# Performance work log

Measured on AMD Instinct MI355X. Metric: run time of the kernel, lower is better.

Reference implementation:

```python
import jax, jax.numpy as jnp
import numpy as np

IN_FEATURES = 8192
OUT_FEATURES = 28672
BATCH = 8  # tokens; skinny GEMM -> memory-bound weight streaming


def setup_inputs() -> dict:
    key = jax.random.key(0)
    k1, k2, k3, k4 = jax.random.split(key, 4)
    x = jax.random.normal(k1, (BATCH, IN_FEATURES), dtype=jnp.float32)
    # ternary codes in {0,1,2} -> weight values {-1,0,+1}; pack 4 codes / byte
    codes = jax.random.randint(k2, (OUT_FEATURES, IN_FEATURES), 0, 3, dtype=jnp.int32)
    codes4 = codes.reshape(OUT_FEATURES, IN_FEATURES // 4, 4)
    shifts = jnp.array([0, 2, 4, 6], dtype=jnp.int32)
    packed_weight = jnp.sum(codes4 << shifts, axis=-1).astype(jnp.int32)  # [O, I//4]
    weight_scale = jax.random.uniform(k3, (1,), dtype=jnp.float32, minval=0.01, maxval=0.1)
    bias = jax.random.normal(k4, (OUT_FEATURES,), dtype=jnp.float32)
    return {"x": x, "packed_weight": packed_weight, "weight_scale": weight_scale, "bias": bias}


def _unpack_ternary(packed):
    # [O, I//4] int -> [O, I] ternary in {-1,0,1}
    shifts = jnp.array([0, 2, 4, 6], dtype=jnp.int32)
    w = ((packed[:, :, None] >> shifts) & 3) - 1  # [O, I//4, 4]
    return w.reshape(packed.shape[0], -1)


def reference(x, packed_weight, weight_scale, bias):
    B = x.shape[0]
    x_flat = x.reshape(B, IN_FEATURES)
    # per-tensor absmax int8 activation quantization
    absmax = jnp.maximum(jnp.max(jnp.abs(x_flat)), 1e-5)
    act_scale = absmax / 127.0
    x_q = jnp.clip(jnp.round(x_flat / act_scale), -128, 127)  # int8 values, kept f32
    w = _unpack_ternary(packed_weight).astype(jnp.float32)  # [O, I]
    # fused dequant GEMM: integer-valued accumulation, single scalar scale
    acc = jnp.einsum('bi,oi->bo', x_q, w)  # exact in f32 (|acc| << 2^24)
    scale = weight_scale[0] * act_scale
    out = acc * scale + bias
    return out.reshape(B, OUT_FEATURES)
```

## Files before the change

kernel.cpp:

```cpp
#include <hip/hip_runtime.h>
#include <stdint.h>

#define O_FEATS 28672
#define I_FEATS 8192
#define BATCH 8

typedef int i32x4 __attribute__((ext_vector_type(4)));


static __device__ __forceinline__ int unpack4(uint32_t p) {
  uint32_t lo = p & 0x0Fu;
  uint32_t hi = (p >> 4) & 0x0Fu;
  uint32_t a = (lo * 0x41u) & 0x0303u;
  uint32_t b = (hi * 0x41u) & 0x0303u;
  return (int)(a | (b << 16));
}

__global__ void k_absmax(const float* __restrict__ x, uint32_t* __restrict__ ws) {
  __shared__ float red[4];
  int t = threadIdx.x;
  float4 v = ((const float4*)x)[blockIdx.x * 256 + t];
  float m = fmaxf(fmaxf(fabsf(v.x), fabsf(v.y)), fmaxf(fabsf(v.z), fabsf(v.w)));
#pragma unroll
  for (int off = 32; off; off >>= 1)
    m = fmaxf(m, __shfl_xor(m, off));
  if ((t & 63) == 0) red[t >> 6] = m;
  __syncthreads();
  if (t == 0)
    ws[16 + blockIdx.x] =
        __float_as_uint(fmaxf(fmaxf(red[0], red[1]), fmaxf(red[2], red[3])));
}

__global__ void k_quant(const float* __restrict__ x, uint32_t* __restrict__ ws) {
  __shared__ float s_amax;
  __shared__ int reds[4];
  int t = threadIdx.x;
  if (blockIdx.x >= 64) {
    int row = 8 + ((blockIdx.x - 64) >> 3), seg = blockIdx.x & 7;
    int k0 = seg * 1024 + t * 4;
    int S = k0 >> 6, g = (k0 >> 4) & 3, j = k0 & 15;
    ws[1024 + ((S * 1024 + (g * 16 + row) * 16 + j) >> 2)] = 0u;
    return;
  }
  int b = blockIdx.x >> 3, seg = blockIdx.x & 7;
  if (t < 64) {
    float m = __uint_as_float(ws[16 + t]);
#pragma unroll
    for (int off = 32; off; off >>= 1)
      m = fmaxf(m, __shfl_xor(m, off));
    if (t == 0) {
      float a = fmaxf(m, 1e-5f);
      s_amax = a;
      ws[0] = __float_as_uint(a);
    }
  }
  __syncthreads();
  float s = s_amax / 127.0f;
  float4 v = ((const float4*)(x + b * I_FEATS + seg * 1024))[t];
  int q0 = (int)fminf(fmaxf(rintf(v.x / s), -128.f), 127.f);
  int q1 = (int)fminf(fmaxf(rintf(v.y / s), -128.f), 127.f);
  int q2 = (int)fminf(fmaxf(rintf(v.z / s), -128.f), 127.f);
  int q3 = (int)fminf(fmaxf(rintf(v.w / s), -128.f), 127.f);
  uint32_t pk = (uint32_t)(q0 & 0xff) | ((uint32_t)(q1 & 0xff) << 8) |
                ((uint32_t)(q2 & 0xff) << 16) | ((uint32_t)(q3 & 0xff) << 24);
  {
    int k0 = seg * 1024 + t * 4;
    int S = k0 >> 6, g = (k0 >> 4) & 3, j = k0 & 15;
    ws[1024 + ((S * 1024 + (g * 16 + b) * 16 + j) >> 2)] = pk;
  }
  int s4 = q0 + q1 + q2 + q3;
#pragma unroll
  for (int off = 32; off; off >>= 1)
    s4 += __shfl_xor(s4, off);
  if ((t & 63) == 0) reds[t >> 6] = s4;
  __syncthreads();
  if (t == 0)
    ws[128 + blockIdx.x] = (uint32_t)(reds[0] + reds[1] + reds[2] + reds[3]);
}

__global__ void __launch_bounds__(256, 4)
k_gemm(const int* __restrict__ Wp, const float* __restrict__ wscale,
       const float* __restrict__ bias, const uint32_t* __restrict__ ws,
       float* __restrict__ out) {
  __shared__ int red[4][32][4];
  __shared__ int s_sumx[BATCH];
  __shared__ float s_scale;

  const int t = threadIdx.x;
  const int wave = t >> 6, lane = t & 63;

  if (t < 64) {
    int p = (int)ws[128 + t];
    p += __shfl_xor(p, 1);
    p += __shfl_xor(p, 2);
    p += __shfl_xor(p, 4);
    if ((t & 7) == 0) s_sumx[t >> 3] = p;
    if (t == 0) s_scale = (__uint_as_float(ws[0]) / 127.0f) * wscale[0];
  }

  const int o_base = blockIdx.x * 16;
  const int m = lane & 15, g = lane >> 4;

  const uint8_t* xqT = (const uint8_t*)(ws + 1024);
  const int4* ap = (const int4*)(xqT + (size_t)(wave * 32) * 1024 + lane * 16);
  const int4* wp = (const int4*)((const uint8_t*)Wp + (size_t)(o_base + m) * 8192 +
                                 wave * 2048 + g * 16);

  i32x4 acc = {0, 0, 0, 0};
  int4 abuf[4], bbuf[4];
#pragma unroll
  for (int i = 0; i < 4; ++i) {
    abuf[i] = ap[i * 64];
    bbuf[i] = wp[i * 4];
  }
#pragma unroll
  for (int s = 0; s < 32; ++s) {
    int4 a = abuf[s & 3];
    int4 b = bbuf[s & 3];
    if (s + 4 < 32) {
      abuf[s & 3] = ap[(s + 4) * 64];
      bbuf[s & 3] = wp[(s + 4) * 4];
    }
    i32x4 af, bf;
    af.x = a.x; af.y = a.y; af.z = a.z; af.w = a.w;
    bf.x = unpack4((uint32_t)b.x);
    bf.y = unpack4((uint32_t)b.y);
    bf.z = unpack4((uint32_t)b.z);
    bf.w = unpack4((uint32_t)b.w);
    acc = __builtin_amdgcn_mfma_i32_16x16x64_i8(af, bf, acc, 0, 0, 0);
  }

  if (lane < 32) {
#pragma unroll
    for (int r = 0; r < 4; ++r) red[wave][lane][r] = acc[r];
  }
  __syncthreads();

  if (t < 32) {
    const int n = t & 15;
    const int q = t >> 4;
    const int o = o_base + n;
    const float bo = bias[o];
#pragma unroll
    for (int r = 0; r < 4; ++r) {
      int mm = q * 4 + r;
      int tot = red[0][t][r] + red[1][t][r] + red[2][t][r] + red[3][t][r];
      out[mm * O_FEATS + o] = (float)(tot - s_sumx[mm]) * s_scale + bo;
    }
  }
}

extern "C" void kernel_launch(void* const* d_in, const int* in_sizes, int n_in,
                              void* d_out, int out_size, void* d_ws, size_t ws_size,
                              hipStream_t stream) {
  const float* x = (const float*)d_in[0];
  const int* pw = (const int*)d_in[1];
  const float* wscale = (const float*)d_in[2];
  const float* bias = (const float*)d_in[3];
  float* out = (float*)d_out;
  uint32_t* ws = (uint32_t*)d_ws;

  k_absmax<<<64, 256, 0, stream>>>(x, ws);
  k_quant<<<128, 256, 0, stream>>>(x, ws);
  k_gemm<<<O_FEATS / 16, 256, 0, stream>>>(pw, wscale, bias, ws, out);
}
```

Measured before the change: 327.8 us.

## Make GEMM persistent with async global-to-LDS double-buffered weight streaming

The GEMM now launches 256 persistent blocks instead of 1792. Each block walks 7 output tiles and streams weight rows into a double-buffered LDS area with global_load_lds. Activations are loaded into registers once per block and reused across tiles, and hand-written waitcnt/barrier asm overlaps the loads with the MFMA work. The cost is lower occupancy (launch bounds of 1, large LDS use, 32 int4 registers) and half the MFMA lanes fed zeros, with latency hiding left to the block's own pipeline.

After: 349.1 us. 6.5% more time.

```diff
diff --git a/kernel.cpp b/kernel.cpp
--- a/kernel.cpp
+++ b/kernel.cpp
@@ -4,8 +4,15 @@
 #define O_FEATS 28672
 #define I_FEATS 8192
 #define BATCH 8
+#define PITCH_WB 8208
+#define HALF_B (8 * PITCH_WB)
 
 typedef int i32x4 __attribute__((ext_vector_type(4)));
+
+#define BAR_VM16 asm volatile("s_waitcnt vmcnt(16)\n\ts_barrier" ::: "memory")
+#define BAR_VM0  asm volatile("s_waitcnt vmcnt(0)\n\ts_barrier" ::: "memory")
+#define BAR_LGKM asm volatile("s_waitcnt lgkmcnt(0)\n\ts_barrier" ::: "memory")
+#define BAR_ONLY asm volatile("s_barrier" ::: "memory")
 
 
 static __device__ __forceinline__ int unpack4(uint32_t p) {
@@ -78,10 +85,11 @@
     ws[128 + blockIdx.x] = (uint32_t)(reds[0] + reds[1] + reds[2] + reds[3]);
 }
 
-__global__ void __launch_bounds__(256, 4)
+__global__ void __launch_bounds__(256, 1)
 k_gemm(const int* __restrict__ Wp, const float* __restrict__ wscale,
        const float* __restrict__ bias, const uint32_t* __restrict__ ws,
        float* __restrict__ out) {
+  __shared__ uint32_t Wlds[2 * 8 * (PITCH_WB / 4)];
   __shared__ int red[4][32][4];
   __shared__ int s_sumx[BATCH];
   __shared__ float s_scale;
@@ -97,56 +105,102 @@
     if ((t & 7) == 0) s_sumx[t >> 3] = p;
     if (t == 0) s_scale = (__uint_as_float(ws[0]) / 127.0f) * wscale[0];
   }
-
-  const int o_base = blockIdx.x * 16;
-  const int m = lane & 15, g = lane >> 4;
+  __syncthreads();
+
+  const uint8_t* W8 = (const uint8_t*)Wp;
+  uint8_t* L8 = (uint8_t*)Wlds;
+
+  {
+    const uint8_t* gs = W8 + (size_t)(blockIdx.x * 16 + 2 * wave) * 8192 + lane * 16;
+    uint32_t* ld = (uint32_t*)(L8 + 2 * wave * PITCH_WB);
+#pragma unroll
+    for (int i = 0; i < 16; ++i)
+      __builtin_amdgcn_global_load_lds(
+          (const uint32_t*)(gs + i * 1024),
+          ld + ((i >> 3) * PITCH_WB + (i & 7) * 1024) / 4, 16, 0, 0);
+  }
 
   const uint8_t* xqT = (const uint8_t*)(ws + 1024);
-  const int4* ap = (const int4*)(xqT + (size_t)(wave * 32) * 1024 + lane * 16);
-  const int4* wp = (const int4*)((const uint8_t*)Wp + (size_t)(o_base + m) * 8192 +
-                                 wave * 2048 + g * 16);
-
-  i32x4 acc = {0, 0, 0, 0};
-  int4 abuf[4], bbuf[4];
-#pragma unroll
-  for (int i = 0; i < 4; ++i) {
-    abuf[i] = ap[i * 64];
-    bbuf[i] = wp[i * 4];
-  }
-#pragma unroll
-  for (int s = 0; s < 32; ++s) {
-    int4 a = abuf[s & 3];
-    int4 b = bbuf[s & 3];
-    if (s + 4 < 32) {
-      abuf[s & 3] = ap[(s + 4) * 64];
-      bbuf[s & 3] = wp[(s + 4) * 4];
-    }
-    i32x4 af, bf;
-    af.x = a.x; af.y = a.y; af.z = a.z; af.w = a.w;
-    bf.x = unpack4((uint32_t)b.x);
-    bf.y = unpack4((uint32_t)b.y);
-    bf.z = unpack4((uint32_t)b.z);
-    bf.w = unpack4((uint32_t)b.w);
-    acc = __builtin_amdgcn_mfma_i32_16x16x64_i8(af, bf, acc, 0, 0, 0);
-  }
-
-  if (lane < 32) {
-#pragma unroll
-    for (int r = 0; r < 4; ++r) red[wave][lane][r] = acc[r];
-  }
-  __syncthreads();
-
-  if (t < 32) {
-    const int n = t & 15;
-    const int q = t >> 4;
-    const int o = o_base + n;
-    const float bo = bias[o];
-#pragma unroll
-    for (int r = 0; r < 4; ++r) {
-      int mm = q * 4 + r;
-      int tot = red[0][t][r] + red[1][t][r] + red[2][t][r] + red[3][t][r];
-      out[mm * O_FEATS + o] = (float)(tot - s_sumx[mm]) * s_scale + bo;
-    }
+  int4 a[32];
+#pragma unroll
+  for (int s = 0; s < 32; ++s)
+    a[s] = *(const int4*)(xqT + (size_t)(wave * 32 + s) * 1024 + lane * 16);
+
+  const int r8 = lane & 7, g = lane >> 4;
+  const bool act0 = ((lane >> 3) & 1) == 0;
+
+  const uint8_t* fr0 = L8 + r8 * PITCH_WB + wave * 2048 + g * 16;
+  const uint8_t* fr1 = L8 + HALF_B + r8 * PITCH_WB + wave * 2048 + g * 16;
+
+  for (int i = 0; i < 7; ++i) {
+    i32x4 acc = {0, 0, 0, 0};
+
+    {
+      const uint8_t* gs =
+          W8 + (size_t)((blockIdx.x + 256 * i) * 16 + 8 + 2 * wave) * 8192 + lane * 16;
+      uint32_t* ld = (uint32_t*)(L8 + HALF_B + 2 * wave * PITCH_WB);
+#pragma unroll
+      for (int k = 0; k < 16; ++k)
+        __builtin_amdgcn_global_load_lds(
+            (const uint32_t*)(gs + k * 1024),
+            ld + ((k >> 3) * PITCH_WB + (k & 7) * 1024) / 4, 16, 0, 0);
+    }
+    BAR_VM16;
+#pragma unroll
+    for (int s = 0; s < 32; ++s) {
+      int4 bw = *(const int4*)(fr0 + s * 64);
+      i32x4 bf, af;
+      bf.x = act0 ? unpack4((uint32_t)bw.x) : 0;
+      bf.y = act0 ? unpack4((uint32_t)bw.y) : 0;
+      bf.z = act0 ? unpack4((uint32_t)bw.z) : 0;
+      bf.w = act0 ? unpack4((uint32_t)bw.w) : 0;
+      af.x = a[s].x; af.y = a[s].y; af.z = a[s].z; af.w = a[s].w;
+      acc = __builtin_amdgcn_mfma_i32_16x16x64_i8(af, bf, acc, 0, 0, 0);
+    }
+    BAR_LGKM;
+
+    if (i < 6) {
+      const uint8_t* gs =
+          W8 + (size_t)((blockIdx.x + 256 * (i + 1)) * 16 + 2 * wave) * 8192 + lane * 16;
+      uint32_t* ld = (uint32_t*)(L8 + 2 * wave * PITCH_WB);
+#pragma unroll
+      for (int k = 0; k < 16; ++k)
+        __builtin_amdgcn_global_load_lds(
+            (const uint32_t*)(gs + k * 1024),
+            ld + ((k >> 3) * PITCH_WB + (k & 7) * 1024) / 4, 16, 0, 0);
+      BAR_VM16;
+    } else {
+      BAR_VM0;
+    }
+#pragma unroll
+    for (int s = 0; s < 32; ++s) {
+      int4 bw = *(const int4*)(fr1 + s * 64);
+      i32x4 bf, af;
+      bf.x = act0 ? 0 : unpack4((uint32_t)bw.x);
+      bf.y = act0 ? 0 : unpack4((uint32_t)bw.y);
+      bf.z = act0 ? 0 : unpack4((uint32_t)bw.z);
+      bf.w = act0 ? 0 : unpack4((uint32_t)bw.w);
+      af.x = a[s].x; af.y = a[s].y; af.z = a[s].z; af.w = a[s].w;
+      acc = __builtin_amdgcn_mfma_i32_16x16x64_i8(af, bf, acc, 0, 0, 0);
+    }
+
+    if (lane < 32) {
+#pragma unroll
+      for (int r = 0; r < 4; ++r) red[wave][lane][r] = acc[r];
+    }
+    BAR_LGKM;
+    if (t < 32) {
+      const int n = t & 15, q = t >> 4;
+      const int o = (blockIdx.x + 256 * i) * 16 + n;
+      const float bo = bias[o];
+#pragma unroll
+      for (int r = 0; r < 4; ++r) {
+        int mm = q * 4 + r;
+        int tot = red[0][t][r] + red[1][t][r] + red[2][t][r] + red[3][t][r];
+        out[mm * O_FEATS + o] = (float)(tot - s_sumx[mm]) * s_scale + bo;
+      }
+    }
+    BAR_ONLY;
   }
 }
 
@@ -162,5 +216,5 @@
 
   k_absmax<<<64, 256, 0, stream>>>(x, ws);
   k_quant<<<128, 256, 0, stream>>>(x, ws);
-  k_gemm<<<O_FEATS / 16, 256, 0, stream>>>(pw, wscale, bias, ws, out);
-}
+  k_gemm<<<256, 256, 0, stream>>>(pw, wscale, bias, ws, out);
+}
```
